# Optimization experiments

Hardware: AMD Instinct MI355X
Metric: run time of the kernel (lower is better)

Reference implementation:

```python
import jax, jax.numpy as jnp
import numpy as np
from jax import lax

B, C, T, P = 32, 8, 65536, 16  # batch, channels, time, filter order


def setup_inputs() -> dict:
    key = jax.random.key(0)
    kx, ka = jax.random.split(key)
    x = jax.random.normal(kx, (B, C, T), dtype=jnp.float32)
    # denominator coeffs a: shape (B, C, P+1). a[...,0]=1, small tails for stability
    a_tail = 0.03 * jax.random.normal(ka, (B, C, P), dtype=jnp.float32)
    a = jnp.concatenate([jnp.ones((B, C, 1), dtype=jnp.float32), a_tail], axis=-1)
    return {"x": x, "a": a}


def _allpole(x, a):
    # y[t] = x[t] - sum_{k=1..p} a_k * y[t-k], with a normalized by a[...,0]
    a_n = a / a[..., 0:1]
    p = a.shape[-1] - 1
    # buffer holds last p outputs oldest->newest; pair with [a_p, ..., a_1]
    a_rev = jnp.flip(a_n[..., 1:], axis=-1)  # (B, C, p)

    def step(buf, x_t):
        # buf: (B, C, p), x_t: (B, C)
        y_t = x_t - jnp.sum(a_rev * buf, axis=-1)
        buf = jnp.concatenate([buf[..., 1:], y_t[..., None]], axis=-1)
        return buf, y_t

    x_time = jnp.moveaxis(x, -1, 0)  # (T, B, C)
    buf0 = jnp.zeros(x.shape[:-1] + (p,), dtype=x.dtype)
    _, ys = lax.scan(step, buf0, x_time)
    return jnp.moveaxis(ys, 0, -1)  # (B, C, T)


def reference(x, a):
    return _allpole(x, a)
```

## Files before the change

### kernel.cpp

```cpp
#include <hip/hip_runtime.h>


constexpr int B_ = 32;
constexpr int C_ = 8;
constexpr int T_ = 65536;
constexpr int P_ = 16;
constexpr int BC = B_ * C_;
constexpr int L_ = 64;
constexpr int W_ = 320;
constexpr int NCHUNK = T_ / L_;
constexpr int BLOCK = 256;
constexpr int CHUNKS_PER_BLK = BLOCK;
constexpr int BLKS_PER_CH = NCHUNK / CHUNKS_PER_BLK;
constexpr int NBLOCKS = BC * BLKS_PER_CH;
constexpr int NSTAGE = CHUNKS_PER_BLK * L_ + W_;
constexpr int NUNITS = NSTAGE / 4;
constexpr int NUNITS_PAD = NUNITS + NUNITS / 16;

__device__ __forceinline__ float f4c(const float4& v, int c) {
    switch (c & 3) {
        case 0:  return v.x;
        case 1:  return v.y;
        case 2:  return v.z;
        default: return v.w;
    }
}

#define STEPB(P)                                                          \
    _Pragma("unroll")                                                     \
    for (int s = 0; s < 16; ++s) {                                        \
        float acc = f4c((P)[s >> 2], s);                                  \
        _Pragma("unroll")                                                 \
        for (int k = 16; k >= 2; --k)                                     \
            acc = fmaf(b[k], h[(s - k) & 15], acc);                       \
        h[s] = fmaf(b[1], h[(s - 1) & 15], acc);                          \
    }

#define STEPO(P, OS)                                                      \
    _Pragma("unroll")                                                     \
    for (int s = 0; s < 16; ++s) {                                        \
        float acc = f4c((P)[s >> 2], s);                                  \
        _Pragma("unroll")                                                 \
        for (int k = 16; k >= 2; --k)                                     \
            acc = fmaf(b[k], h[(s - k) & 15], acc);                       \
        h[s] = fmaf(b[1], h[(s - 1) & 15], acc);                          \
        (OS)[s] = h[s];                                                   \
    }

#define LDSRD(P, i) do {                                                  \
        const int ru_ = (tid << 4) + ((i) << 2);                          \
        const int pu_ = ru_ + (ru_ >> 4);                                 \
        (P)[0] = lds4[pu_ + 0]; (P)[1] = lds4[pu_ + 1];                   \
        (P)[2] = lds4[pu_ + 2]; (P)[3] = lds4[pu_ + 3];                   \
    } while (0)

__global__ __launch_bounds__(BLOCK, 2) void allpole_kernel(
    const float* __restrict__ x, const float* __restrict__ a,
    float* __restrict__ y)
{
    __shared__ float4 lds4[NUNITS_PAD];

    const int tid = threadIdx.x;
    const int blk = blockIdx.x;
    const int ch  = blk >> 2;
    const int ci0 = (blk & (BLKS_PER_CH - 1)) * CHUNKS_PER_BLK;
    const int ci  = ci0 + tid;

    const float* __restrict__ xc = x + (size_t)ch * T_;
    float* __restrict__ yc       = y + (size_t)ch * T_;
    const float* __restrict__ ac = a + ch * (P_ + 1);

    const int xbase = ci0 * L_ - W_;
    for (int u = tid; u < NUNITS; u += BLOCK) {
        const int af = xbase + u * 4;
        float4 v;
        if (af >= 0) v = *reinterpret_cast<const float4*>(xc + af);
        else { v.x = 0.0f; v.y = 0.0f; v.z = 0.0f; v.w = 0.0f; }
        lds4[u + (u >> 4)] = v;
    }

    const float inv_a0 = 1.0f / ac[0];
    float b[P_ + 1];
#pragma unroll
    for (int k = 1; k <= P_; ++k) b[k] = -ac[k] * inv_a0;

    float h[16];
#pragma unroll
    for (int i = 0; i < 16; ++i) h[i] = 0.0f;

    __syncthreads();

    float4 pA[4], pB[4], pC[4];
    LDSRD(pA, 0);
    LDSRD(pB, 1);

#pragma unroll 1
    for (int it = 0; it < 18; it += 3) {
        LDSRD(pC, it + 2);  STEPB(pA)
        LDSRD(pA, it + 3);  STEPB(pB)
        LDSRD(pB, it + 4);  STEPB(pC)
    }
    LDSRD(pC, 20);  STEPB(pA)
    LDSRD(pA, 21);  STEPB(pB)

    const int obase = ci * L_;
    float os[16];
    LDSRD(pB, 22);  STEPO(pC, os)
    LDSRD(pC, 23);  STEPB(pA)
#pragma unroll
    for (int q = 0; q < 4; ++q) {
        float4 v;
        v.x = os[q * 4 + 0]; v.y = os[q * 4 + 1];
        v.z = os[q * 4 + 2]; v.w = os[q * 4 + 3];
        *reinterpret_cast<float4*>(yc + obase + q * 4) = v;
    }
#pragma unroll
    for (int q = 0; q < 4; ++q) {
        float4 v;
        v.x = h[q * 4 + 0]; v.y = h[q * 4 + 1];
        v.z = h[q * 4 + 2]; v.w = h[q * 4 + 3];
        *reinterpret_cast<float4*>(yc + obase + 16 + q * 4) = v;
    }
    STEPO(pB, os)
    STEPB(pC)
#pragma unroll
    for (int q = 0; q < 4; ++q) {
        float4 v;
        v.x = os[q * 4 + 0]; v.y = os[q * 4 + 1];
        v.z = os[q * 4 + 2]; v.w = os[q * 4 + 3];
        *reinterpret_cast<float4*>(yc + obase + 32 + q * 4) = v;
    }
#pragma unroll
    for (int q = 0; q < 4; ++q) {
        float4 v;
        v.x = h[q * 4 + 0]; v.y = h[q * 4 + 1];
        v.z = h[q * 4 + 2]; v.w = h[q * 4 + 3];
        *reinterpret_cast<float4*>(yc + obase + 48 + q * 4) = v;
    }
}

extern "C" void kernel_launch(void* const* d_in, const int* in_sizes, int n_in,
                              void* d_out, int out_size, void* d_ws, size_t ws_size,
                              hipStream_t stream) {
    const float* x = (const float*)d_in[0];
    const float* a = (const float*)d_in[1];
    float* y = (float*)d_out;
    allpole_kernel<<<NBLOCKS, BLOCK, 0, stream>>>(x, a, y);
}
```

Baseline: 151.7 us.

## Double chunk length to cut warmup overhead and split recurrence into parallel partial sums

Each thread now owns a 128-sample chunk instead of 64, with the same 320-sample warmup, so the redundant warmup work per output sample shrinks while the total thread count halves (128-thread blocks, launch bounds minimum 1). The 16-tap recurrence is restructured into four independent partial accumulators summed in a tree, shortening the serial FMA dependency chain per output sample. LDS padding and the index math are changed to a stride of 32 units. The risk is fewer waves for latency hiding (half as many threads) and slightly different rounding from reassociating the sum.

```diff
diff --git a/kernel.cpp b/kernel.cpp
--- a/kernel.cpp
+++ b/kernel.cpp
@@ -6,16 +6,16 @@
 constexpr int T_ = 65536;
 constexpr int P_ = 16;
 constexpr int BC = B_ * C_;
-constexpr int L_ = 64;
+constexpr int L_ = 128;
 constexpr int W_ = 320;
 constexpr int NCHUNK = T_ / L_;
-constexpr int BLOCK = 256;
+constexpr int BLOCK = 128;
 constexpr int CHUNKS_PER_BLK = BLOCK;
 constexpr int BLKS_PER_CH = NCHUNK / CHUNKS_PER_BLK;
 constexpr int NBLOCKS = BC * BLKS_PER_CH;
 constexpr int NSTAGE = CHUNKS_PER_BLK * L_ + W_;
 constexpr int NUNITS = NSTAGE / 4;
-constexpr int NUNITS_PAD = NUNITS + NUNITS / 16;
+constexpr int NUNITS_PAD = NUNITS + (NUNITS >> 5) + 1;
 
 __device__ __forceinline__ float f4c(const float4& v, int c) {
     switch (c & 3) {
@@ -29,32 +29,66 @@
 #define STEPB(P)                                                          \
     _Pragma("unroll")                                                     \
     for (int s = 0; s < 16; ++s) {                                        \
-        float acc = f4c((P)[s >> 2], s);                                  \
-        _Pragma("unroll")                                                 \
-        for (int k = 16; k >= 2; --k)                                     \
-            acc = fmaf(b[k], h[(s - k) & 15], acc);                       \
-        h[s] = fmaf(b[1], h[(s - 1) & 15], acc);                          \
+        float c0 = fmaf(b[2],  h[(s - 2)  & 15], f4c((P)[s >> 2], s));    \
+        c0 = fmaf(b[3],  h[(s - 3)  & 15], c0);                           \
+        c0 = fmaf(b[4],  h[(s - 4)  & 15], c0);                           \
+        c0 = fmaf(b[5],  h[(s - 5)  & 15], c0);                           \
+        float c1 = b[6] * h[(s - 6)  & 15];                               \
+        c1 = fmaf(b[7],  h[(s - 7)  & 15], c1);                           \
+        c1 = fmaf(b[8],  h[(s - 8)  & 15], c1);                           \
+        c1 = fmaf(b[9],  h[(s - 9)  & 15], c1);                           \
+        float c2 = b[10] * h[(s - 10) & 15];                              \
+        c2 = fmaf(b[11], h[(s - 11) & 15], c2);                           \
+        c2 = fmaf(b[12], h[(s - 12) & 15], c2);                           \
+        c2 = fmaf(b[13], h[(s - 13) & 15], c2);                           \
+        float c3 = b[14] * h[(s - 14) & 15];                              \
+        c3 = fmaf(b[15], h[(s - 15) & 15], c3);                           \
+        c3 = fmaf(b[16], h[(s - 16) & 15], c3);                           \
+        const float pre = (c0 + c1) + (c2 + c3);                          \
+        h[s] = fmaf(b[1], h[(s - 1) & 15], pre);                          \
     }
 
 #define STEPO(P, OS)                                                      \
     _Pragma("unroll")                                                     \
     for (int s = 0; s < 16; ++s) {                                        \
-        float acc = f4c((P)[s >> 2], s);                                  \
-        _Pragma("unroll")                                                 \
-        for (int k = 16; k >= 2; --k)                                     \
-            acc = fmaf(b[k], h[(s - k) & 15], acc);                       \
-        h[s] = fmaf(b[1], h[(s - 1) & 15], acc);                          \
+        float c0 = fmaf(b[2],  h[(s - 2)  & 15], f4c((P)[s >> 2], s));    \
+        c0 = fmaf(b[3],  h[(s - 3)  & 15], c0);                           \
+        c0 = fmaf(b[4],  h[(s - 4)  & 15], c0);                           \
+        c0 = fmaf(b[5],  h[(s - 5)  & 15], c0);                           \
+        float c1 = b[6] * h[(s - 6)  & 15];                               \
+        c1 = fmaf(b[7],  h[(s - 7)  & 15], c1);                           \
+        c1 = fmaf(b[8],  h[(s - 8)  & 15], c1);                           \
+        c1 = fmaf(b[9],  h[(s - 9)  & 15], c1);                           \
+        float c2 = b[10] * h[(s - 10) & 15];                              \
+        c2 = fmaf(b[11], h[(s - 11) & 15], c2);                           \
+        c2 = fmaf(b[12], h[(s - 12) & 15], c2);                           \
+        c2 = fmaf(b[13], h[(s - 13) & 15], c2);                           \
+        float c3 = b[14] * h[(s - 14) & 15];                              \
+        c3 = fmaf(b[15], h[(s - 15) & 15], c3);                           \
+        c3 = fmaf(b[16], h[(s - 16) & 15], c3);                           \
+        const float pre = (c0 + c1) + (c2 + c3);                          \
+        h[s] = fmaf(b[1], h[(s - 1) & 15], pre);                          \
         (OS)[s] = h[s];                                                   \
     }
 
 #define LDSRD(P, i) do {                                                  \
-        const int ru_ = (tid << 4) + ((i) << 2);                          \
-        const int pu_ = ru_ + (ru_ >> 4);                                 \
+        const int ru_ = (tid << 5) + ((i) << 2);                          \
+        const int pu_ = ru_ + (ru_ >> 5);                                 \
         (P)[0] = lds4[pu_ + 0]; (P)[1] = lds4[pu_ + 1];                   \
         (P)[2] = lds4[pu_ + 2]; (P)[3] = lds4[pu_ + 3];                   \
     } while (0)
 
-__global__ __launch_bounds__(BLOCK, 2) void allpole_kernel(
+#define STORE16(OFS, SRC) do {                                            \
+        _Pragma("unroll")                                                 \
+        for (int q = 0; q < 4; ++q) {                                     \
+            float4 v;                                                     \
+            v.x = (SRC)[q * 4 + 0]; v.y = (SRC)[q * 4 + 1];               \
+            v.z = (SRC)[q * 4 + 2]; v.w = (SRC)[q * 4 + 3];               \
+            *reinterpret_cast<float4*>(yc + obase + (OFS) + q * 4) = v;   \
+        }                                                                 \
+    } while (0)
+
+__global__ __launch_bounds__(BLOCK, 1) void allpole_kernel(
     const float* __restrict__ x, const float* __restrict__ a,
     float* __restrict__ y)
 {
@@ -76,7 +110,7 @@
         float4 v;
         if (af >= 0) v = *reinterpret_cast<const float4*>(xc + af);
         else { v.x = 0.0f; v.y = 0.0f; v.z = 0.0f; v.w = 0.0f; }
-        lds4[u + (u >> 4)] = v;
+        lds4[u + (u >> 5)] = v;
     }
 
     const float inv_a0 = 1.0f / ac[0];
@@ -105,38 +139,22 @@
 
     const int obase = ci * L_;
     float os[16];
+
     LDSRD(pB, 22);  STEPO(pC, os)
     LDSRD(pC, 23);  STEPB(pA)
-#pragma unroll
-    for (int q = 0; q < 4; ++q) {
-        float4 v;
-        v.x = os[q * 4 + 0]; v.y = os[q * 4 + 1];
-        v.z = os[q * 4 + 2]; v.w = os[q * 4 + 3];
-        *reinterpret_cast<float4*>(yc + obase + q * 4) = v;
-    }
-#pragma unroll
-    for (int q = 0; q < 4; ++q) {
-        float4 v;
-        v.x = h[q * 4 + 0]; v.y = h[q * 4 + 1];
-        v.z = h[q * 4 + 2]; v.w = h[q * 4 + 3];
-        *reinterpret_cast<float4*>(yc + obase + 16 + q * 4) = v;
-    }
-    STEPO(pB, os)
-    STEPB(pC)
-#pragma unroll
-    for (int q = 0; q < 4; ++q) {
-        float4 v;
-        v.x = os[q * 4 + 0]; v.y = os[q * 4 + 1];
-        v.z = os[q * 4 + 2]; v.w = os[q * 4 + 3];
-        *reinterpret_cast<float4*>(yc + obase + 32 + q * 4) = v;
-    }
-#pragma unroll
-    for (int q = 0; q < 4; ++q) {
-        float4 v;
-        v.x = h[q * 4 + 0]; v.y = h[q * 4 + 1];
-        v.z = h[q * 4 + 2]; v.w = h[q * 4 + 3];
-        *reinterpret_cast<float4*>(yc + obase + 48 + q * 4) = v;
-    }
+    STORE16(0, os); STORE16(16, h);
+
+    LDSRD(pA, 24);  STEPO(pB, os)
+    LDSRD(pB, 25);  STEPB(pC)
+    STORE16(32, os); STORE16(48, h);
+
+    LDSRD(pC, 26);  STEPO(pA, os)
+    LDSRD(pA, 27);  STEPB(pB)
+    STORE16(64, os); STORE16(80, h);
+
+    STEPO(pC, os)
+    STEPB(pA)
+    STORE16(96, os); STORE16(112, h);
 }
 
 extern "C" void kernel_launch(void* const* d_in, const int* in_sizes, int n_in,
```

New measurement: 168.0 us. +10.7%, slower.
